# Performance work log

Hardware: AMD Instinct MI355X
Metric: run time of the kernel (lower is better)

Reference implementation:

```python
import jax, jax.numpy as jnp
import numpy as np

B, S, BERT_H = 8, 512, 432
NL, HD = 12, 64
H = NL * HD  # 768
NEG = -1e12

def _lin(k, i, o):
    return jax.random.normal(k, (i, o), jnp.float32) * 0.02

def setup_inputs():
    key = jax.random.key(0)
    ks = jax.random.split(key, 12)
    return {
        "bert_hidden": jax.random.normal(ks[0], (B, S, BERT_H), jnp.float32),
        "attention_mask": jnp.ones((B, S), jnp.float32),
        "dense_w": _lin(ks[1], BERT_H, H), "dense_b": jnp.zeros((H,)),
        "sat_qw": _lin(ks[2], H, H), "sat_qb": jnp.zeros((H,)),
        "sat_kw": _lin(ks[3], H, H), "sat_kb": jnp.zeros((H,)),
        "sat_vw": _lin(ks[4], H, H), "sat_vb": jnp.zeros((H,)),
        "sat_ow": _lin(ks[5], H, H), "sat_ob": jnp.zeros((H,)),
        "rel_qw": _lin(ks[6], H, H), "rel_qb": jnp.zeros((H,)),
        "rel_kw": _lin(ks[7], H, H), "rel_kb": jnp.zeros((H,)),
        "rel_vw": _lin(ks[8], H, H), "rel_vb": jnp.zeros((H,)),
        "rel_ow": _lin(ks[9], H, H), "rel_ob": jnp.zeros((H,)),
        "lns_w": jnp.ones((H,)), "lns_b": jnp.zeros((H,)),
        "lnr_w": jnp.ones((H,)), "lnr_b": jnp.zeros((H,)),
        "head_w": _lin(ks[10], H, 2 * HD), "head_b": jnp.zeros((2 * HD,)),
        "tail_w": _lin(ks[11], 2 * HD, 2 * NL), "tail_b": jnp.zeros((2 * NL,)),
    }

def _layernorm(x, w, b, eps=1e-12):
    u = x.mean(-1, keepdims=True)
    s = ((x - u) ** 2).mean(-1, keepdims=True)
    return w * (x - u) / jnp.sqrt(s + eps) + b

def _mha(q_in, k_in, v_in, wq, bq, wk, bk, wv, bv, wo, bo):
    # q_in: [N, Lq, H]; k_in/v_in: [N, Lk, H]; dropout is identity (eval)
    N, Lq, _ = q_in.shape
    Lk = k_in.shape[1]
    qh = (q_in @ wq + bq).reshape(N, Lq, NL, HD)
    kh = (k_in @ wk + bk).reshape(N, Lk, NL, HD)
    vh = (v_in @ wv + bv).reshape(N, Lk, NL, HD)
    scores = jnp.einsum('nqhd,nkhd->nhqk', qh, kh) / np.float32(np.sqrt(HD))
    probs = jax.nn.softmax(scores, axis=-1)
    ctx = jnp.einsum('nhqk,nkhd->nqhd', probs, vh).reshape(N, Lq, NL * HD)
    return ctx @ wo + bo + q_in

def _shift_back(x):
    # faithful torch cycle_shift(forward=False): circular roll left by 1
    return jnp.roll(x, -1, axis=1)

def _shift_fwd(x):
    # faithful to the torch sequential in-place loop in cycle_shift(forward=True):
    # out[0] = x[-1]; out[1:] = x[0] (each copy reads the already-overwritten slot)
    b, s, h = x.shape
    return jnp.concatenate([x[:, -1:, :], jnp.broadcast_to(x[:, :1, :], (b, s - 1, h))], axis=1)

def reference(bert_hidden, attention_mask, dense_w, dense_b,
              sat_qw, sat_qb, sat_kw, sat_kb, sat_vw, sat_vb, sat_ow, sat_ob,
              rel_qw, rel_qb, rel_kw, rel_kb, rel_vw, rel_vb, rel_ow, rel_ob,
              lns_w, lns_b, lnr_w, lnr_b, head_w, head_b, tail_w, tail_b):
    hidden0 = bert_hidden @ dense_w + dense_b  # [B,S,H]
    cs = hidden0
    center = cs.mean(axis=1)  # [B,H], avg_pool2d over seq dim
    for _ in range(2):
        before = _shift_back(cs)
        after = _shift_fwd(cs)
        center_exp = jnp.broadcast_to(center[:, None, :], cs.shape)
        concats = jnp.stack([before, cs, after, hidden0, center_exp], axis=2)  # [B,S,5,H]
        concats = concats.reshape(B * S, 5, H)
        q = cs.reshape(B * S, 1, H)
        sat = _mha(q, concats, concats, sat_qw, sat_qb, sat_kw, sat_kb, sat_vw, sat_vb, sat_ow, sat_ob)
        cs = _layernorm(jax.nn.relu(sat), lns_w, lns_b).reshape(B, S, H)
        cc = jnp.concatenate([center[:, None, :], cs], axis=1)  # [B,S+1,H]
        rel = _mha(center[:, None, :], cc, cc, rel_qw, rel_qb, rel_kw, rel_kb, rel_vw, rel_vb, rel_ow, rel_ob)
        center = _layernorm(jax.nn.relu(rel), lnr_w, lnr_b)[:, 0, :]
    outputs = cs @ head_w + head_b  # [B,S,2*HD]
    qw, kw = outputs[..., ::2], outputs[..., 1::2]  # [B,S,HD]
    pos = jnp.arange(S, dtype=jnp.float32)
    inv = jnp.power(10000.0, -2.0 * jnp.arange(HD // 2, dtype=jnp.float32) / HD)
    ang = pos[:, None] * inv[None, :]  # [S,HD//2]
    pe = jnp.stack([jnp.sin(ang), jnp.cos(ang)], axis=-1).reshape(S, HD)
    cos_pos = jnp.repeat(pe[:, 1::2], 2, axis=-1)  # [S,HD]
    sin_pos = jnp.repeat(pe[:, ::2], 2, axis=-1)
    def rot(x):
        x2 = jnp.stack([-x[..., 1::2], x[..., ::2]], axis=-1).reshape(x.shape)
        return x * cos_pos + x2 * sin_pos
    qw, kw = rot(qw), rot(kw)
    logits = jnp.einsum('bmd,bnd->bmn', qw, kw) / np.float32(np.sqrt(HD))  # [B,S,S]
    bias = jnp.einsum('bnh->bhn', outputs @ tail_w + tail_b) / 2.0  # [B,2*NL,S]
    logits = logits[:, None, :, :] + bias[:, ::2, None, :] + bias[:, 1::2, :, None]  # [B,NL,S,S]
    m1 = attention_mask[:, None, :, None]
    logits = logits * m1 + NEG * (1.0 - m1)
    m2 = attention_mask[:, None, None, :]
    logits = logits * m2 + NEG * (1.0 - m2)
    tril = jnp.tril(jnp.ones((S, S), logits.dtype), k=-1)
    return logits - tril * 1e12
```

## Files before the change

kernel.cpp:

```cpp
#include <hip/hip_runtime.h>
#include <cstdint>
#include <cstddef>

#define HH 768
#define SS 512
#define NBATCH 8
#define NLH 12
#define HDIM 64
#define BSROWS 4096
static constexpr float NEGV = -1000000000000.0f;

typedef unsigned short ushort_t;
typedef __attribute__((ext_vector_type(4))) float fx4;
typedef __attribute__((ext_vector_type(8))) short sx8;

__device__ __forceinline__ ushort_t f2bf(float f) {
  uint32_t u = __float_as_uint(f);
  uint32_t r = (u + 0x7FFFu + ((u >> 16) & 1u)) >> 16;
  return (ushort_t)r;
}
__device__ __forceinline__ float bf2f(ushort_t h) {
  return __uint_as_float(((uint32_t)h) << 16);
}
__device__ __forceinline__ float2 ldbf2(const ushort_t* p) {
  uint32_t u = *(const uint32_t*)p;
  return make_float2(__uint_as_float(u << 16), __uint_as_float(u & 0xffff0000u));
}

__device__ __forceinline__ void async_copy16(void* lds, const void* g) {
  __builtin_amdgcn_global_load_lds(
      (const __attribute__((address_space(1))) void*)g,
      (__attribute__((address_space(3))) void*)lds, 16, 0, 0);
}

__device__ __forceinline__ void gemm_core(
    char* arena, int bid, int nwg, int nx,
    const ushort_t* __restrict__ A, int lda,
    const ushort_t* __restrict__ B, int ldb,
    const float* __restrict__ bias,
    const ushort_t* __restrict__ resb,
    ushort_t* __restrict__ Cb, int ldo,
    ushort_t* __restrict__ Cb2, int ldo2, int nsplit, int K,
    float* __restrict__ colmean)
{
  ushort_t* As = (ushort_t*)arena;
  ushort_t* Bs = (ushort_t*)(arena + 16384);
  const int tid = threadIdx.x;
  const int q = nwg >> 3;
  const int xcd = bid & 7, sidx = bid >> 3;
  const int swz = xcd * q + sidx;
  const int bm = (swz / nx) * 128;
  const int bn = (swz % nx) * 128;
  const int l = tid & 63;
  const int w = tid >> 6;
  const int wr = w >> 1, wc = w & 1;
  const int r8 = tid >> 3;
  const int sl = tid & 7;

  fx4 acc[4][4];
#pragma unroll
  for (int m = 0; m < 4; ++m)
#pragma unroll
    for (int n = 0; n < 4; ++n) acc[m][n] = (fx4)0.f;

  for (int k0 = 0; k0 < K; k0 += 64) {
#pragma unroll
    for (int i = 0; i < 4; ++i) {
      int row = i * 32 + r8;
      int srcs = sl ^ (row & 7);
      async_copy16((char*)As + i * 4096 + tid * 16,
                   A + (size_t)(bm + row) * lda + k0 + srcs * 8);
    }
#pragma unroll
    for (int i = 0; i < 4; ++i) {
      int row = i * 32 + r8;
      int srcs = sl ^ (row & 7);
      async_copy16((char*)Bs + i * 4096 + tid * 16,
                   B + (size_t)(bn + row) * ldb + k0 + srcs * 8);
    }
    __syncthreads();
#pragma unroll
    for (int kk = 0; kk < 2; ++kk) {
      sx8 av[4], bv[4];
      const int so = (l >> 4) + kk * 4;
#pragma unroll
      for (int m = 0; m < 4; ++m) {
        int r = wr * 64 + m * 16 + (l & 15);
        av[m] = *(const sx8*)((const char*)As + r * 128 + ((so ^ (r & 7)) * 16));
      }
#pragma unroll
      for (int n = 0; n < 4; ++n) {
        int r = wc * 64 + n * 16 + (l & 15);
        bv[n] = *(const sx8*)((const char*)Bs + r * 128 + ((so ^ (r & 7)) * 16));
      }
#pragma unroll
      for (int m = 0; m < 4; ++m)
#pragma unroll
        for (int n = 0; n < 4; ++n)
          acc[m][n] = __builtin_amdgcn_mfma_f32_16x16x32_bf16(av[m], bv[n], acc[m][n], 0, 0, 0);
    }
    __syncthreads();
  }

  const bool second = (bn >= nsplit);
  ushort_t* dst = second ? Cb2 : Cb;
  const int ld = second ? ldo2 : ldo;
  const int csub = second ? nsplit : 0;
  const int cr0 = bm + wr * 64 + (l >> 4) * 4;
  const int cc0 = bn + wc * 64 + (l & 15);
#pragma unroll
  for (int m = 0; m < 4; ++m) {
#pragma unroll
    for (int n = 0; n < 4; ++n) {
      int col = cc0 + n * 16;
      float bcol = bias[col];
#pragma unroll
      for (int j = 0; j < 4; ++j) {
        int row = cr0 + m * 16 + j;
        size_t off = (size_t)row * ld + (col - csub);
        float v = acc[m][n][j] + bcol;
        if (resb) v += bf2f(resb[off]);
        dst[off] = f2bf(v);
      }
    }
  }

  if (colmean) {
    float* scr = (float*)arena;
    const int cid = wr * 4 + (l >> 4);
#pragma unroll
    for (int n = 0; n < 4; ++n) {
      int colL = wc * 64 + n * 16 + (l & 15);
      float t = 16.0f * bias[bn + colL];
#pragma unroll
      for (int m = 0; m < 4; ++m)
#pragma unroll
        for (int j = 0; j < 4; ++j) t += acc[m][n][j];
      scr[cid * 128 + colL] = t;
    }
    __syncthreads();
    if (tid < 128) {
      float scol = 0.f;
#pragma unroll
      for (int c = 0; c < 8; ++c) scol += scr[c * 128 + tid];
      atomicAdd(&colmean[(bm >> 9) * HH + bn + tid], scol * (1.0f / 512.0f));
    }
  }
}

struct SmallJob { const float* W; const float* bias; const float* res; float* C; };
struct SmallJobs { SmallJob j[5]; };

__device__ __forceinline__ void skinny_core(
    char* arena, int colblk,
    const float* __restrict__ A, const float* __restrict__ W,
    const float* __restrict__ bias, const float* __restrict__ res, float* __restrict__ C)
{
  float* As = (float*)arena;
  float* part = (float*)(arena + 24576);
  const int tid = threadIdx.x;
#pragma unroll
  for (int i = 0; i < 6; ++i) {
    int idx = tid * 4 + i * 1024;
    *(float4*)&As[idx] = *(const float4*)(A + idx);
  }
  __syncthreads();
  const int c = tid & 31;
  const int col = (colblk << 5) + c;
  const int ks = tid >> 5;
  const float* Wp = W + (size_t)(ks * 96) * HH + col;
  float acc[8] = {};
#pragma unroll 8
  for (int k = 0; k < 96; ++k) {
    float wv = Wp[(size_t)k * HH];
    const float* ap = &As[ks * 96 + k];
#pragma unroll
    for (int m = 0; m < 8; ++m)
      acc[m] = fmaf(ap[m * HH], wv, acc[m]);
  }
#pragma unroll
  for (int m = 0; m < 8; ++m)
    part[ks * 256 + m * 32 + c] = acc[m];
  __syncthreads();
  const int m = tid >> 5;
  const int c2 = tid & 31;
  float s = 0.f;
#pragma unroll
  for (int k = 0; k < 8; ++k) s += part[k * 256 + m * 32 + c2];
  const int outcol = (colblk << 5) + c2;
  float v = s + bias[outcol];
  if (res) v += res[(size_t)m * HH + outcol];
  C[(size_t)m * HH + outcol] = v;
}

__device__ __forceinline__ void rel_core(
    char* arena, int b, int h,
    const float* __restrict__ Qr, const float* __restrict__ Krc, const ushort_t* __restrict__ Kr,
    const float* __restrict__ Vrc, const ushort_t* __restrict__ Vr,
    const float* __restrict__ rel_ow, float* __restrict__ relo)
{
  float* qs = (float*)arena;
  float* sc = (float*)(arena + 256);
  float* part = (float*)(arena + 2560);
  float* redm = (float*)(arena + 3584);
  float* redsum = (float*)(arena + 3600);
  float* ctxs = (float*)(arena + 3616);
  int t = threadIdx.x, lane = t & 63, wave = t >> 6;
  if (t < 64) qs[t] = Qr[b * HH + h * HDIM + t];
  __syncthreads();
  for (int j = t; j < 513; j += 256) {
    float acc = 0.f;
    if (j == 0) {
      const float* kp = Krc + b * HH + h * HDIM;
#pragma unroll
      for (int d = 0; d < HDIM; ++d) acc = fmaf(qs[d], kp[d], acc);
    } else {
      const sx8* kv = (const sx8*)(Kr + (size_t)(b * SS + j - 1) * 1536 + h * HDIM);
#pragma unroll
      for (int dq = 0; dq < 8; ++dq) {
        sx8 v = kv[dq];
#pragma unroll
        for (int e = 0; e < 8; ++e)
          acc = fmaf(qs[dq * 8 + e], bf2f((ushort_t)v[e]), acc);
      }
    }
    sc[j] = acc * 0.125f;
  }
  __syncthreads();
  float m = -1e30f;
  for (int j = t; j < 513; j += 256) m = fmaxf(m, sc[j]);
#pragma unroll
  for (int d = 1; d < 64; d <<= 1) m = fmaxf(m, __shfl_xor(m, d));
  if (lane == 0) redm[wave] = m;
  __syncthreads();
  m = fmaxf(fmaxf(redm[0], redm[1]), fmaxf(redm[2], redm[3]));
  float lsum = 0.f;
  for (int j = t; j < 513; j += 256) { float e = __expf(sc[j] - m); sc[j] = e; lsum += e; }
#pragma unroll
  for (int d = 1; d < 64; d <<= 1) lsum += __shfl_xor(lsum, d);
  if (lane == 0) redsum[wave] = lsum;
  __syncthreads();
  float total = redsum[0] + redsum[1] + redsum[2] + redsum[3];
  float accv = 0.f;
#pragma unroll 8
  for (int j = wave; j < 513; j += 4) {
    float vv = (j == 0) ? Vrc[b * HH + h * HDIM + lane]
                        : bf2f(Vr[(size_t)(b * SS + j - 1) * 1536 + h * HDIM + lane]);
    accv = fmaf(sc[j], vv, accv);
  }
  part[wave * 64 + lane] = accv;
  __syncthreads();
  if (wave == 0)
    ctxs[lane] = (part[0 * 64 + lane] + part[1 * 64 + lane] +
                  part[2 * 64 + lane] + part[3 * 64 + lane]) / total;
  __syncthreads();
  for (int c = t; c < HH; c += 256) {
    const float* Wp = rel_ow + (size_t)(h * 64) * HH + c;
    float a0 = 0.f, a1 = 0.f, a2 = 0.f, a3 = 0.f;
#pragma unroll
    for (int d = 0; d < 64; d += 4) {
      a0 = fmaf(ctxs[d + 0], Wp[(size_t)(d + 0) * HH], a0);
      a1 = fmaf(ctxs[d + 1], Wp[(size_t)(d + 1) * HH], a1);
      a2 = fmaf(ctxs[d + 2], Wp[(size_t)(d + 2) * HH], a2);
      a3 = fmaf(ctxs[d + 3], Wp[(size_t)(d + 3) * HH], a3);
    }
    atomicAdd(&relo[b * HH + c], (a0 + a1) + (a2 + a3));
  }
}

__global__ __launch_bounds__(256) void gemm_bf16(
    const ushort_t* __restrict__ A, int lda,
    const ushort_t* __restrict__ B, int ldb,
    const float* __restrict__ bias,
    const ushort_t* __restrict__ resb,
    ushort_t* __restrict__ Cb, int ldo,
    ushort_t* __restrict__ Cb2, int ldo2, int nsplit, int K, int nx,
    float* __restrict__ colmean)
{
  __shared__ char arena[32768];
  gemm_core(arena, blockIdx.x, gridDim.x, nx, A, lda, B, ldb, bias, resb,
            Cb, ldo, Cb2, ldo2, nsplit, K, colmean);
}

__global__ __launch_bounds__(256) void qkv_center(
    const ushort_t* __restrict__ A, const ushort_t* __restrict__ B,
    const float* __restrict__ bias, ushort_t* __restrict__ Cb,
    SmallJobs jobs, const float* __restrict__ center)
{
  __shared__ char arena[32768];
  if (blockIdx.x < 576) {
    gemm_core(arena, blockIdx.x, 576, 18, A, HH, B, HH, bias, nullptr,
              Cb, 2304, nullptr, 0, 1 << 30, HH, nullptr);
  } else {
    int vb = blockIdx.x - 576;
    SmallJob jb = jobs.j[vb / 24];
    skinny_core(arena, vb % 24, center, jb.W, jb.bias, jb.res, jb.C);
  }
}

__global__ __launch_bounds__(256) void qkv2_rel(
    const ushort_t* __restrict__ A, const ushort_t* __restrict__ B,
    const float* __restrict__ bias, ushort_t* __restrict__ Cb,
    const float* __restrict__ Qr, const float* __restrict__ Krc,
    const ushort_t* __restrict__ Kr,
    const float* __restrict__ Vrc, const ushort_t* __restrict__ Vr,
    const float* __restrict__ rel_ow, float* __restrict__ relo)
{
  __shared__ char arena[32768];
  if (blockIdx.x < 576) {
    gemm_core(arena, blockIdx.x, 576, 18, A, HH, B, HH, bias, nullptr,
              Cb, 2304, nullptr, 0, 1 << 30, HH, nullptr);
  } else {
    int v = blockIdx.x - 576;
    rel_core(arena, v / 12, v % 12, Qr, Krc, Kr, Vrc, Vr, rel_ow, relo);
  }
}

struct SmallJobs2 { SmallJob j[2]; };
__global__ __launch_bounds__(256) void skinny_ln(
    const float* __restrict__ relo, const float* __restrict__ rel_ob,
    const float* __restrict__ center,
    const float* __restrict__ lw, const float* __restrict__ lb,
    SmallJobs2 jobs)
{
  __shared__ float As[8 * HH];
  __shared__ float part[8 * 8 * 32];
  const int tid = threadIdx.x;
  const SmallJob job = jobs.j[blockIdx.y];
#pragma unroll
  for (int i = 0; i < 6; ++i) {
    int idx = tid * 4 + i * 1024;
    int row = idx / HH;
    int col = idx - row * HH;
    float4 r4 = *(const float4*)(relo + idx);
    float4 o4 = *(const float4*)(rel_ob + col);
    float4 c4 = *(const float4*)(center + idx);
    As[idx + 0] = r4.x + o4.x + c4.x;
    As[idx + 1] = r4.y + o4.y + c4.y;
    As[idx + 2] = r4.z + o4.z + c4.z;
    As[idx + 3] = r4.w + o4.w + c4.w;
  }
  __syncthreads();
  {
    const int row = tid >> 5, lc = tid & 31;
    float s = 0.f, sq = 0.f;
#pragma unroll
    for (int e = 0; e < 24; ++e) {
      float x = fmaxf(As[row * HH + lc * 24 + e], 0.f);
      s += x; sq += x * x;
    }
#pragma unroll
    for (int d = 1; d < 32; d <<= 1) { s += __shfl_xor(s, d); sq += __shfl_xor(sq, d); }
    float mean = s * (1.0f / HH);
    float var = sq * (1.0f / HH) - mean * mean;
    float rstd = rsqrtf(var + 1e-12f);
#pragma unroll
    for (int e = 0; e < 24; ++e) {
      int cc = lc * 24 + e;
      float x = fmaxf(As[row * HH + cc], 0.f);
      As[row * HH + cc] = lw[cc] * (x - mean) * rstd + lb[cc];
    }
  }
  __syncthreads();
  const int c = tid & 31;
  const int col = (blockIdx.x << 5) + c;
  const int ks = tid >> 5;
  const float* Wp = job.W + (size_t)(ks * 96) * HH + col;
  float acc[8] = {};
#pragma unroll 8
  for (int k = 0; k < 96; ++k) {
    float wv = Wp[(size_t)k * HH];
    const float* ap = &As[ks * 96 + k];
#pragma unroll
    for (int m = 0; m < 8; ++m)
      acc[m] = fmaf(ap[m * HH], wv, acc[m]);
  }
#pragma unroll
  for (int m = 0; m < 8; ++m)
    part[ks * 256 + m * 32 + c] = acc[m];
  __syncthreads();
  const int m = tid >> 5;
  const int c2 = tid & 31;
  float s2 = 0.f;
#pragma unroll
  for (int k = 0; k < 8; ++k) s2 += part[k * 256 + m * 32 + c2];
  const int outcol = (blockIdx.x << 5) + c2;
  job.C[(size_t)m * HH + outcol] = s2 + job.bias[outcol];
}

__global__ __launch_bounds__(256) void head_fused(
    const ushort_t* __restrict__ Araw,
    const float* __restrict__ lnw, const float* __restrict__ lnb,
    const ushort_t* __restrict__ B,
    const float* __restrict__ head_b,
    const float* __restrict__ tail_w,
    const float* __restrict__ tail_b,
    float* __restrict__ qw, float* __restrict__ kw,
    float* __restrict__ bias2)
{
  __shared__ ushort_t As[16 * 64];
  __shared__ ushort_t Bs[128 * 64];
  __shared__ float tile[16][130];
  __shared__ float invt[32];
  __shared__ float2 rst[16];
  const int tid = threadIdx.x;
  const int bm = blockIdx.x * 16;
  const int l = tid & 63;
  const int w = tid >> 6;
  const int r8 = tid >> 3;
  const int sl = tid & 7;

  if (tid < 32) invt[tid] = powf(10000.0f, -(float)tid / 32.0f);

  {
    int row = tid >> 4, part = tid & 15;
    const ushort_t* rp = Araw + (size_t)(bm + row) * HH + part * 48;
    float s = 0.f, sq = 0.f;
#pragma unroll
    for (int c = 0; c < 6; ++c) {
      sx8 v = *(const sx8*)(rp + c * 8);
#pragma unroll
      for (int e = 0; e < 8; ++e) {
        float x = fmaxf(bf2f((ushort_t)v[e]), 0.f);
        s += x; sq += x * x;
      }
    }
#pragma unroll
    for (int d = 1; d < 16; d <<= 1) { s += __shfl_xor(s, d); sq += __shfl_xor(sq, d); }
    if (part == 0) {
      float mean = s * (1.0f / HH);
      float var = sq * (1.0f / HH) - mean * mean;
      rst[row] = make_float2(mean, rsqrtf(var + 1e-12f));
    }
  }
  __syncthreads();

  fx4 acc[2];
  acc[0] = (fx4)0.f; acc[1] = (fx4)0.f;

  for (int k0 = 0; k0 < HH; k0 += 64) {
#pragma unroll
    for (int i = 0; i < 4; ++i) {
      int row = i * 32 + r8;
      int srcs = sl ^ (row & 7);
      async_copy16((char*)Bs + i * 4096 + tid * 16,
                   B + (size_t)row * HH + k0 + srcs * 8);
    }
    if (tid < 128) {
      int row = tid >> 3;
      int slot = sl ^ (row & 7);
      int gk = k0 + slot * 8;
      sx8 v = *(const sx8*)(Araw + (size_t)(bm + row) * HH + gk);
      float4 w0 = *(const float4*)(lnw + gk);
      float4 w1 = *(const float4*)(lnw + gk + 4);
      float4 b0 = *(const float4*)(lnb + gk);
      float4 b1 = *(const float4*)(lnb + gk + 4);
      float wv[8] = {w0.x, w0.y, w0.z, w0.w, w1.x, w1.y, w1.z, w1.w};
      float bv[8] = {b0.x, b0.y, b0.z, b0.w, b1.x, b1.y, b1.z, b1.w};
      float2 mr = rst[row];
      sx8 ov;
#pragma unroll
      for (int e = 0; e < 8; ++e) {
        float x = fmaxf(bf2f((ushort_t)v[e]), 0.f);
        ov[e] = (short)f2bf(fmaf((x - mr.x) * mr.y, wv[e], bv[e]));
      }
      *(sx8*)((char*)As + row * 128 + sl * 16) = ov;
    }
    __syncthreads();
#pragma unroll
    for (int kk = 0; kk < 2; ++kk) {
      const int so = (l >> 4) + kk * 4;
      int ra = l & 15;
      sx8 av = *(const sx8*)((const char*)As + ra * 128 + ((so ^ (ra & 7)) * 16));
#pragma unroll
      for (int n = 0; n < 2; ++n) {
        int r = w * 32 + n * 16 + (l & 15);
        sx8 bv = *(const sx8*)((const char*)Bs + r * 128 + ((so ^ (r & 7)) * 16));
        acc[n] = __builtin_amdgcn_mfma_f32_16x16x32_bf16(av, bv, acc[n], 0, 0, 0);
      }
    }
    __syncthreads();
  }

  {
    const int rr0 = (l >> 4) * 4;
#pragma unroll
    for (int n = 0; n < 2; ++n) {
      int col = w * 32 + n * 16 + (l & 15);
      float bcol = head_b[col];
#pragma unroll
      for (int j = 0; j < 4; ++j)
        tile[rr0 + j][col] = acc[n][j] + bcol;
    }
  }
  __syncthreads();

#pragma unroll
  for (int it = 0; it < 2; ++it) {
    int t = tid + it * 256;
    int r = t >> 5, i = t & 31;
    int s = (bm + r) & 511;
    float ang = (float)s * invt[i];
    float sn = sinf(ang), cn = cosf(ang);
    float q0 = tile[r][4 * i + 0], k0 = tile[r][4 * i + 1];
    float q1 = tile[r][4 * i + 2], k1 = tile[r][4 * i + 3];
    float* qp = qw + (size_t)(bm + r) * 64 + i * 2;
    float* kp = kw + (size_t)(bm + r) * 64 + i * 2;
    qp[0] = q0 * cn - q1 * sn; qp[1] = q1 * cn + q0 * sn;
    kp[0] = k0 * cn - k1 * sn; kp[1] = k1 * cn + k0 * sn;
  }
  for (int t = tid; t < 16 * 24; t += 256) {
    int r = t / 24, c = t % 24;
    float acc2 = tail_b[c];
#pragma unroll 16
    for (int k = 0; k < 128; ++k) acc2 = fmaf(tile[r][k], tail_w[k * 24 + c], acc2);
    bias2[(size_t)(bm + r) * 24 + c] = acc2 * 0.5f;
  }
}

struct TJob { const float* src; ushort_t* dst; int K, N, Kpad, rowOff; };
struct PrepArgs {
  TJob j[8];
  const float* bert; ushort_t* bert_bf;
  const float* rkb; const float* rvb; const float* sqb; const float* skb; const float* svb;
  float* b_merged;
  float* center;
  float* relo;
};
__global__ __launch_bounds__(256) void prep_all(PrepArgs pa)
{
  if (blockIdx.z < 8) {
    TJob jb = pa.j[blockIdx.z];
    int k0 = blockIdx.x * 32, n0 = blockIdx.y * 32;
    if (k0 >= jb.Kpad || n0 >= jb.N) return;
    __shared__ float t[32][33];
    int tx = threadIdx.x & 31, ty = threadIdx.x >> 5;
#pragma unroll
    for (int i = 0; i < 4; ++i) {
      int k = k0 + ty + i * 8;
      float v = 0.f;
      if (k < jb.K && n0 + tx < jb.N) v = jb.src[(size_t)k * jb.N + n0 + tx];
      t[ty + i * 8][tx] = v;
    }
    __syncthreads();
#pragma unroll
    for (int i = 0; i < 4; ++i) {
      int n = n0 + ty + i * 8;
      int k = k0 + tx;
      if (n < jb.N && k < jb.Kpad)
        jb.dst[(size_t)(jb.rowOff + n) * jb.Kpad + k] = f2bf(t[tx][ty + i * 8]);
    }
  } else {
    const int NB = BSROWS * 448;
    const int total = NB + 3840 + 2 * NBATCH * HH;
    int start = (blockIdx.y * 24 + blockIdx.x) * 256 + threadIdx.x;
    for (int i = start; i < total; i += 24 * 24 * 256) {
      if (i < NB) {
        int r = i / 448, c = i % 448;
        pa.bert_bf[i] = (c < 432) ? f2bf(pa.bert[(size_t)r * 432 + c]) : (ushort_t)0;
      } else if (i < NB + 3840) {
        int c = i - NB;
        float v;
        if (c < 768) v = pa.rkb[c];
        else if (c < 1536) v = pa.rvb[c - 768];
        else if (c < 2304) v = pa.sqb[c - 1536];
        else if (c < 3072) v = pa.skb[c - 2304];
        else v = pa.svb[c - 3072];
        pa.b_merged[c] = v;
      } else if (i < NB + 3840 + NBATCH * HH) {
        pa.center[i - NB - 3840] = 0.f;
      } else {
        pa.relo[i - NB - 3840 - NBATCH * HH] = 0.f;
      }
    }
  }
}

__global__ __launch_bounds__(256) void sat_attn(
    const ushort_t* __restrict__ Qc, const ushort_t* __restrict__ Kc,
    const ushort_t* __restrict__ Vc, int ldq,
    const ushort_t* __restrict__ Kh0, const ushort_t* __restrict__ Vh0, int ldh,
    const float* __restrict__ Kcen, const float* __restrict__ Vcen,
    ushort_t* __restrict__ ctxb)
{
  int i = ((blockIdx.x & 7) << 9) | (blockIdx.x >> 3);
  int b = i >> 9, s = i & 511;
  int lane = threadIdx.x & 63;
  int wave = threadIdx.x >> 6;
  size_t rb = (size_t)(b * SS + ((s + 1) & 511));
  size_t rs = (size_t)i;
  size_t ra = (size_t)(b * SS + (s == 0 ? (SS - 1) : 0));
  size_t rc = (size_t)b * HH;
  const int half = lane >> 5;
  const int d0 = (lane & 31) * 2;
#pragma unroll
  for (int it = 0; it < 2; ++it) {
    int p = wave + 4 * it;
    if (p >= 6) break;
    int off = (2 * p + half) * HDIM + d0;
    float2 q  = ldbf2(Qc + rs * ldq + off);
    float2 kb = ldbf2(Kc + rb * ldq + off);
    float2 ks = ldbf2(Kc + rs * ldq + off);
    float2 ka = ldbf2(Kc + ra * ldq + off);
    float2 kh = ldbf2(Kh0 + rs * ldh + off);
    float2 kc = *(const float2*)(Kcen + rc + off);
    float s0 = q.x * kb.x + q.y * kb.y;
    float s1 = q.x * ks.x + q.y * ks.y;
    float s2 = q.x * ka.x + q.y * ka.y;
    float s3 = q.x * kh.x + q.y * kh.y;
    float s4 = q.x * kc.x + q.y * kc.y;
#pragma unroll
    for (int d = 1; d < 32; d <<= 1) {
      s0 += __shfl_xor(s0, d); s1 += __shfl_xor(s1, d); s2 += __shfl_xor(s2, d);
      s3 += __shfl_xor(s3, d); s4 += __shfl_xor(s4, d);
    }
    const float sc = 0.125f;
    s0 *= sc; s1 *= sc; s2 *= sc; s3 *= sc; s4 *= sc;
    float mx = fmaxf(fmaxf(fmaxf(s0, s1), fmaxf(s2, s3)), s4);
    float e0 = __expf(s0 - mx), e1 = __expf(s1 - mx), e2 = __expf(s2 - mx);
    float e3 = __expf(s3 - mx), e4 = __expf(s4 - mx);
    float inv = 1.f / (e0 + e1 + e2 + e3 + e4);
    float2 vb = ldbf2(Vc + rb * ldq + off);
    float2 vs = ldbf2(Vc + rs * ldq + off);
    float2 va = ldbf2(Vc + ra * ldq + off);
    float2 vh = ldbf2(Vh0 + rs * ldh + off);
    float2 vc = *(const float2*)(Vcen + rc + off);
    float vx = e0 * vb.x + e1 * vs.x + e2 * va.x + e3 * vh.x + e4 * vc.x;
    float vy = e0 * vb.y + e1 * vs.y + e2 * va.y + e3 * vh.y + e4 * vc.y;
    uint32_t o = (uint32_t)f2bf(vx * inv) | ((uint32_t)f2bf(vy * inv) << 16);
    *(uint32_t*)(ctxb + rs * HH + off) = o;
  }
}

__global__ __launch_bounds__(256) void relu_ln_bf(
    const ushort_t* __restrict__ x, const float* __restrict__ w, const float* __restrict__ b,
    ushort_t* __restrict__ ybf)
{
  int row = blockIdx.x;
  const ushort_t* xr = x + (size_t)row * HH;
  float v[3];
  float sum = 0.f, sumsq = 0.f;
#pragma unroll
  for (int j = 0; j < 3; ++j) {
    float t = bf2f(xr[threadIdx.x + j * 256]);
    t = fmaxf(t, 0.f);
    v[j] = t;
    sum += t; sumsq += t * t;
  }
#pragma unroll
  for (int d = 1; d < 64; d <<= 1) { sum += __shfl_xor(sum, d); sumsq += __shfl_xor(sumsq, d); }
  __shared__ float ws_[4], wsq_[4];
  int wave = threadIdx.x >> 6, lane = threadIdx.x & 63;
  if (lane == 0) { ws_[wave] = sum; wsq_[wave] = sumsq; }
  __syncthreads();
  sum = ws_[0] + ws_[1] + ws_[2] + ws_[3];
  sumsq = wsq_[0] + wsq_[1] + wsq_[2] + wsq_[3];
  float mean = sum * (1.0f / HH);
  float var = sumsq * (1.0f / HH) - mean * mean;
  float rstd = rsqrtf(var + 1e-12f);
#pragma unroll
  for (int j = 0; j < 3; ++j) {
    int cidx = threadIdx.x + j * 256;
    float o = w[cidx] * (v[j] - mean) * rstd + b[cidx];
    ybf[(size_t)row * HH + cidx] = f2bf(o);
  }
}

__global__ __launch_bounds__(256) void final_kernel(
    const float* __restrict__ qw, const float* __restrict__ kw,
    const float* __restrict__ bias2, const float* __restrict__ mask,
    float* __restrict__ out)
{
  int b = blockIdx.z;
  int mt = blockIdx.y * 32;
  int nt = blockIdx.x * 32;
  __shared__ float qs[32][68];
  __shared__ float ks[32][68];
  int t = threadIdx.x;
  {
    int idx = t * 8;
    int r = idx >> 6, c = idx & 63;
    const float* sq = qw + (size_t)(b * SS + mt + r) * 64 + c;
    const float* sk = kw + (size_t)(b * SS + nt + r) * 64 + c;
    *(float4*)&qs[r][c]     = *(const float4*)(sq);
    *(float4*)&qs[r][c + 4] = *(const float4*)(sq + 4);
    *(float4*)&ks[r][c]     = *(const float4*)(sk);
    *(float4*)&ks[r][c + 4] = *(const float4*)(sk + 4);
  }
  __syncthreads();
  int m = t >> 3;
  int n0 = (t & 7) * 4;
  float d0 = 0.f, d1 = 0.f, d2 = 0.f, d3 = 0.f;
#pragma unroll
  for (int d = 0; d < 64; d += 4) {
    float4 qv = *(const float4*)&qs[m][d];
    float4 k0 = *(const float4*)&ks[n0 + 0][d];
    float4 k1 = *(const float4*)&ks[n0 + 1][d];
    float4 k2 = *(const float4*)&ks[n0 + 2][d];
    float4 k3 = *(const float4*)&ks[n0 + 3][d];
    d0 += qv.x * k0.x + qv.y * k0.y + qv.z * k0.z + qv.w * k0.w;
    d1 += qv.x * k1.x + qv.y * k1.y + qv.z * k1.z + qv.w * k1.w;
    d2 += qv.x * k2.x + qv.y * k2.y + qv.z * k2.z + qv.w * k2.w;
    d3 += qv.x * k3.x + qv.y * k3.y + qv.z * k3.z + qv.w * k3.w;
  }
  int gm = mt + m;
  int gn = nt + n0;
  d0 *= 0.125f; d1 *= 0.125f; d2 *= 0.125f; d3 *= 0.125f;
  float mm = mask[b * SS + gm];
  float mn0 = mask[b * SS + gn + 0];
  float mn1 = mask[b * SS + gn + 1];
  float mn2 = mask[b * SS + gn + 2];
  float mn3 = mask[b * SS + gn + 3];
  const float* bmp  = bias2 + (size_t)(b * SS + gm) * 24;
  const float* bnp0 = bias2 + (size_t)(b * SS + gn + 0) * 24;
  const float* bnp1 = bias2 + (size_t)(b * SS + gn + 1) * 24;
  const float* bnp2 = bias2 + (size_t)(b * SS + gn + 2) * 24;
  const float* bnp3 = bias2 + (size_t)(b * SS + gn + 3) * 24;
#pragma unroll
  for (int h = 0; h < NLH; ++h) {
    float tb = bmp[2 * h + 1];
    float v0 = d0 + bnp0[2 * h] + tb;
    float v1 = d1 + bnp1[2 * h] + tb;
    float v2 = d2 + bnp2[2 * h] + tb;
    float v3 = d3 + bnp3[2 * h] + tb;
    v0 = v0 * mm + NEGV * (1.f - mm); v1 = v1 * mm + NEGV * (1.f - mm);
    v2 = v2 * mm + NEGV * (1.f - mm); v3 = v3 * mm + NEGV * (1.f - mm);
    v0 = v0 * mn0 + NEGV * (1.f - mn0); v1 = v1 * mn1 + NEGV * (1.f - mn1);
    v2 = v2 * mn2 + NEGV * (1.f - mn2); v3 = v3 * mn3 + NEGV * (1.f - mn3);
    if (gm > gn + 0) v0 -= 1000000000000.0f;
    if (gm > gn + 1) v1 -= 1000000000000.0f;
    if (gm > gn + 2) v2 -= 1000000000000.0f;
    if (gm > gn + 3) v3 -= 1000000000000.0f;
    float4 o = make_float4(v0, v1, v2, v3);
    *(float4*)(out + ((((size_t)(b * NLH + h)) * SS + gm) * SS + gn)) = o;
  }
}

extern "C" void kernel_launch(void* const* d_in, const int* in_sizes, int n_in,
                              void* d_out, int out_size, void* d_ws, size_t ws_size,
                              hipStream_t stream)
{
  const float* bert    = (const float*)d_in[0];
  const float* amask   = (const float*)d_in[1];
  const float* dense_w = (const float*)d_in[2];
  const float* dense_b = (const float*)d_in[3];
  const float* sat_qw  = (const float*)d_in[4];
  const float* sat_qb  = (const float*)d_in[5];
  const float* sat_kw  = (const float*)d_in[6];
  const float* sat_kb  = (const float*)d_in[7];
  const float* sat_vw  = (const float*)d_in[8];
  const float* sat_vb  = (const float*)d_in[9];
  const float* sat_ow  = (const float*)d_in[10];
  const float* sat_ob  = (const float*)d_in[11];
  const float* rel_qw  = (const float*)d_in[12];
  const float* rel_qb  = (const float*)d_in[13];
  const float* rel_kw  = (const float*)d_in[14];
  const float* rel_kb  = (const float*)d_in[15];
  const float* rel_vw  = (const float*)d_in[16];
  const float* rel_vb  = (const float*)d_in[17];
  const float* rel_ow  = (const float*)d_in[18];
  const float* rel_ob  = (const float*)d_in[19];
  const float* lns_w   = (const float*)d_in[20];
  const float* lns_b   = (const float*)d_in[21];
  const float* lnr_w   = (const float*)d_in[22];
  const float* lnr_b   = (const float*)d_in[23];
  const float* head_w  = (const float*)d_in[24];
  const float* head_b  = (const float*)d_in[25];
  const float* tail_w  = (const float*)d_in[26];
  const float* tail_b  = (const float*)d_in[27];

  float* out = (float*)d_out;
  char*  ws  = (char*)d_ws;

  size_t off = 0;
  auto alloc = [&](size_t bytes) { char* p = ws + off; off += (bytes + 255) & ~(size_t)255; return p; };
  ushort_t* bert_bf   = (ushort_t*)alloc((size_t)BSROWS * 448 * 2);
  ushort_t* Wt_dense  = (ushort_t*)alloc((size_t)768 * 448 * 2);
  ushort_t* Wt_big    = (ushort_t*)alloc((size_t)3840 * 768 * 2);
  ushort_t* Wt_satow  = (ushort_t*)alloc((size_t)768 * 768 * 2);
  ushort_t* Wt_head   = (ushort_t*)alloc((size_t)128 * 768 * 2);
  ushort_t* hidden0_bf= (ushort_t*)alloc((size_t)BSROWS * HH * 2);
  ushort_t* ctx_bf    = (ushort_t*)alloc((size_t)BSROWS * HH * 2);
  ushort_t* csA_bf    = (ushort_t*)alloc((size_t)BSROWS * HH * 2);
  float* b_merged = (float*)alloc(3840 * 4);
  float* center   = (float*)alloc(6144 * 4);
  float* Kcen     = (float*)alloc(6144 * 4);
  float* Vcen     = (float*)alloc(6144 * 4);
  float* Qr       = (float*)alloc(6144 * 4);
  float* Krc      = (float*)alloc(6144 * 4);
  float* Vrc      = (float*)alloc(6144 * 4);
  float* relo     = (float*)alloc(6144 * 4);
  float* bias2    = (float*)alloc((size_t)BSROWS * 24 * 4);
  float* qwbuf    = (float*)alloc((size_t)BSROWS * 64 * 4);
  float* kwbuf    = (float*)alloc((size_t)BSROWS * 64 * 4);

  ushort_t* QKV1_bf = (ushort_t*)out;
  ushort_t* tmp1_bf = QKV1_bf + (size_t)BSROWS * 2304;
  ushort_t* KrVr_bf = tmp1_bf + (size_t)BSROWS * 768;
  ushort_t* QKV2_bf = KrVr_bf + (size_t)BSROWS * 1536;
  ushort_t* tmp2_bf = tmp1_bf;

  dim3 blk(256);

  {
    PrepArgs pa;
    pa.j[0] = { dense_w, Wt_dense, 432, 768, 448, 0 };
    pa.j[1] = { rel_kw,  Wt_big,   768, 768, 768, 0 };
    pa.j[2] = { rel_vw,  Wt_big,   768, 768, 768, 768 };
    pa.j[3] = { sat_qw,  Wt_big,   768, 768, 768, 1536 };
    pa.j[4] = { sat_kw,  Wt_big,   768, 768, 768, 2304 };
    pa.j[5] = { sat_vw,  Wt_big,   768, 768, 768, 3072 };
    pa.j[6] = { sat_ow,  Wt_satow, 768, 768, 768, 0 };
    pa.j[7] = { head_w,  Wt_head,  768, 128, 768, 0 };
    pa.bert = bert; pa.bert_bf = bert_bf;
    pa.rkb = rel_kb; pa.rvb = rel_vb; pa.sqb = sat_qb; pa.skb = sat_kb; pa.svb = sat_vb;
    pa.b_merged = b_merged; pa.center = center; pa.relo = relo;
    prep_all<<<dim3(24, 24, 9), blk, 0, stream>>>(pa);
  }

  gemm_bf16<<<dim3(192), blk, 0, stream>>>(bert_bf, 448, Wt_dense, 448, dense_b,
                                           nullptr, hidden0_bf, HH,
                                           nullptr, 0, 1 << 30, 448, 6, center);

  {
    SmallJobs jobs;
    jobs.j[0] = { sat_kw, sat_kb, nullptr, Kcen };
    jobs.j[1] = { sat_vw, sat_vb, nullptr, Vcen };
    jobs.j[2] = { rel_qw, rel_qb, nullptr, Qr };
    jobs.j[3] = { rel_kw, rel_kb, nullptr, Krc };
    jobs.j[4] = { rel_vw, rel_vb, nullptr, Vrc };
    qkv_center<<<dim3(696), blk, 0, stream>>>(hidden0_bf, Wt_big + (size_t)1536 * 768,
                                              b_merged + 1536, QKV1_bf, jobs, center);
  }
  sat_attn<<<BSROWS, 256, 0, stream>>>(QKV1_bf, QKV1_bf + 768, QKV1_bf + 1536, 2304,
                                       QKV1_bf + 768, QKV1_bf + 1536, 2304,
                                       Kcen, Vcen, ctx_bf);
  gemm_bf16<<<dim3(192), blk, 0, stream>>>(ctx_bf, HH, Wt_satow, HH, sat_ob,
                                           hidden0_bf, tmp1_bf, HH,
                                           nullptr, 0, 1 << 30, HH, 6, nullptr);
  relu_ln_bf<<<BSROWS, 256, 0, stream>>>(tmp1_bf, lns_w, lns_b, csA_bf);

  gemm_bf16<<<dim3(480), blk, 0, stream>>>(csA_bf, HH, Wt_big, HH, b_merged,
                                           nullptr, KrVr_bf, 1536,
                                           nullptr, 0, 1 << 30, HH, 12, nullptr);
  qkv2_rel<<<dim3(672), blk, 0, stream>>>(csA_bf, Wt_big + (size_t)1536 * 768,
                                          b_merged + 1536, QKV2_bf,
                                          Qr, Krc, KrVr_bf, Vrc, KrVr_bf + 768,
                                          rel_ow, relo);
  {
    SmallJobs2 jobs;
    jobs.j[0] = { sat_kw, sat_kb, nullptr, Kcen };
    jobs.j[1] = { sat_vw, sat_vb, nullptr, Vcen };
    skinny_ln<<<dim3(24, 2), blk, 0, stream>>>(relo, rel_ob, center, lnr_w, lnr_b, jobs);
  }
  sat_attn<<<BSROWS, 256, 0, stream>>>(QKV2_bf, QKV2_bf + 768, QKV2_bf + 1536, 2304,
                                       QKV1_bf + 768, QKV1_bf + 1536, 2304,
                                       Kcen, Vcen, ctx_bf);
  gemm_bf16<<<dim3(192), blk, 0, stream>>>(ctx_bf, HH, Wt_satow, HH, sat_ob,
                                           csA_bf, tmp2_bf, HH,
                                           nullptr, 0, 1 << 30, HH, 6, nullptr);
  head_fused<<<256, blk, 0, stream>>>(tmp2_bf, lns_w, lns_b, Wt_head, head_b,
                                      tail_w, tail_b, qwbuf, kwbuf, bias2);
  final_kernel<<<dim3(16, 16, 8), 256, 0, stream>>>(qwbuf, kwbuf, bias2, amask, out);
}
```

Baseline: 256.8 us.

## Fold rel K/V projections into query-side vectors, drop KrVr GEMM

Removes the 4096x1536 GEMM that materialised the rel-attention K and V projections. Scores are now computed as cs·(Wk·q) plus a bias term, using a per-(batch,head) folded vector built in extra blocks appended to the first sat_attn launch. The context is computed as (probs·cs)·Wv plus bias corrections. This trades a large MFMA GEMM for scalar dot products over cs inside the rel blocks, which now read the full 768-wide rows and run longer, so those blocks could become the tail of qkv2_rel.

Result: slower. 332.9 us (+29.7%).

```diff
diff --git a/kernel.cpp b/kernel.cpp
--- a/kernel.cpp
+++ b/kernel.cpp
@@ -39,8 +39,7 @@
     const ushort_t* __restrict__ B, int ldb,
     const float* __restrict__ bias,
     const ushort_t* __restrict__ resb,
-    ushort_t* __restrict__ Cb, int ldo,
-    ushort_t* __restrict__ Cb2, int ldo2, int nsplit, int K,
+    ushort_t* __restrict__ Cb, int ldo, int K,
     float* __restrict__ colmean)
 {
   ushort_t* As = (ushort_t*)arena;
@@ -102,10 +101,6 @@
     __syncthreads();
   }
 
-  const bool second = (bn >= nsplit);
-  ushort_t* dst = second ? Cb2 : Cb;
-  const int ld = second ? ldo2 : ldo;
-  const int csub = second ? nsplit : 0;
   const int cr0 = bm + wr * 64 + (l >> 4) * 4;
   const int cc0 = bn + wc * 64 + (l & 15);
 #pragma unroll
@@ -117,10 +112,10 @@
 #pragma unroll
       for (int j = 0; j < 4; ++j) {
         int row = cr0 + m * 16 + j;
-        size_t off = (size_t)row * ld + (col - csub);
+        size_t off = (size_t)row * ldo + col;
         float v = acc[m][n][j] + bcol;
         if (resb) v += bf2f(resb[off]);
-        dst[off] = f2bf(v);
+        Cb[off] = f2bf(v);
       }
     }
   }
@@ -193,76 +188,98 @@
   C[(size_t)m * HH + outcol] = v;
 }
 
-__device__ __forceinline__ void rel_core(
+__device__ __forceinline__ void rel_core2(
     char* arena, int b, int h,
-    const float* __restrict__ Qr, const float* __restrict__ Krc, const ushort_t* __restrict__ Kr,
-    const float* __restrict__ Vrc, const ushort_t* __restrict__ Vr,
+    const ushort_t* __restrict__ cs,
+    const float* __restrict__ wtil, const float* __restrict__ qkb,
+    const float* __restrict__ Qr, const float* __restrict__ Krc,
+    const float* __restrict__ Vrc,
+    const float* __restrict__ rel_vw, const float* __restrict__ rel_vb,
     const float* __restrict__ rel_ow, float* __restrict__ relo)
 {
-  float* qs = (float*)arena;
-  float* sc = (float*)(arena + 256);
-  float* part = (float*)(arena + 2560);
-  float* redm = (float*)(arena + 3584);
-  float* redsum = (float*)(arena + 3600);
-  float* ctxs = (float*)(arena + 3616);
-  int t = threadIdx.x, lane = t & 63, wave = t >> 6;
-  if (t < 64) qs[t] = Qr[b * HH + h * HDIM + t];
-  __syncthreads();
-  for (int j = t; j < 513; j += 256) {
+  float* wt    = (float*)arena;
+  float* p     = (float*)(arena + 3072);
+  float* ctil  = (float*)(arena + 5376);
+  float* red   = (float*)(arena + 8448);
+  float* ctx   = (float*)(arena + 8576);
+  float* part4 = (float*)(arena + 8832);
+  const int tid = threadIdx.x, lane = tid & 63, wave = tid >> 6;
+
+  for (int k = tid; k < HH; k += 256) wt[k] = wtil[(size_t)(b * 12 + h) * HH + k];
+  __syncthreads();
+  const float qk = qkb[b * 12 + h];
+#pragma unroll
+  for (int jj = 0; jj < 2; ++jj) {
+    int j = 1 + tid + jj * 256;
+    const sx8* cp = (const sx8*)(cs + ((size_t)(b * SS) + (j - 1)) * HH);
+    float s0 = 0.f, s1 = 0.f;
+    for (int k8 = 0; k8 < 96; k8 += 2) {
+      sx8 v0 = cp[k8], v1 = cp[k8 + 1];
+#pragma unroll
+      for (int e = 0; e < 8; ++e) {
+        s0 = fmaf(bf2f((ushort_t)v0[e]), wt[k8 * 8 + e], s0);
+        s1 = fmaf(bf2f((ushort_t)v1[e]), wt[k8 * 8 + 8 + e], s1);
+      }
+    }
+    p[j] = s0 + s1 + qk;
+  }
+  if (tid < 64) {
+    float s0 = Qr[b * HH + h * 64 + tid] * Krc[b * HH + h * 64 + tid];
+#pragma unroll
+    for (int d = 1; d < 64; d <<= 1) s0 += __shfl_xor(s0, d);
+    if (tid == 0) p[0] = s0 * 0.125f;
+  }
+  __syncthreads();
+  float m = -1e30f;
+  for (int j = tid; j < 513; j += 256) m = fmaxf(m, p[j]);
+#pragma unroll
+  for (int d = 1; d < 64; d <<= 1) m = fmaxf(m, __shfl_xor(m, d));
+  if (lane == 0) red[wave] = m;
+  __syncthreads();
+  m = fmaxf(fmaxf(red[0], red[1]), fmaxf(red[2], red[3]));
+  float ls = 0.f;
+  for (int j = tid; j < 513; j += 256) { float e = __expf(p[j] - m); p[j] = e; ls += e; }
+#pragma unroll
+  for (int d = 1; d < 64; d <<= 1) ls += __shfl_xor(ls, d);
+  if (lane == 0) red[4 + wave] = ls;
+  __syncthreads();
+  float inv = 1.f / (red[4] + red[5] + red[6] + red[7]);
+  for (int j = tid; j < 513; j += 256) p[j] *= inv;
+  __syncthreads();
+#pragma unroll
+  for (int kk = 0; kk < 3; ++kk) {
+    int k = tid + kk * 256;
     float acc = 0.f;
-    if (j == 0) {
-      const float* kp = Krc + b * HH + h * HDIM;
-#pragma unroll
-      for (int d = 0; d < HDIM; ++d) acc = fmaf(qs[d], kp[d], acc);
-    } else {
-      const sx8* kv = (const sx8*)(Kr + (size_t)(b * SS + j - 1) * 1536 + h * HDIM);
-#pragma unroll
-      for (int dq = 0; dq < 8; ++dq) {
-        sx8 v = kv[dq];
-#pragma unroll
-        for (int e = 0; e < 8; ++e)
-          acc = fmaf(qs[dq * 8 + e], bf2f((ushort_t)v[e]), acc);
-      }
-    }
-    sc[j] = acc * 0.125f;
-  }
-  __syncthreads();
-  float m = -1e30f;
-  for (int j = t; j < 513; j += 256) m = fmaxf(m, sc[j]);
-#pragma unroll
-  for (int d = 1; d < 64; d <<= 1) m = fmaxf(m, __shfl_xor(m, d));
-  if (lane == 0) redm[wave] = m;
-  __syncthreads();
-  m = fmaxf(fmaxf(redm[0], redm[1]), fmaxf(redm[2], redm[3]));
-  float lsum = 0.f;
-  for (int j = t; j < 513; j += 256) { float e = __expf(sc[j] - m); sc[j] = e; lsum += e; }
-#pragma unroll
-  for (int d = 1; d < 64; d <<= 1) lsum += __shfl_xor(lsum, d);
-  if (lane == 0) redsum[wave] = lsum;
-  __syncthreads();
-  float total = redsum[0] + redsum[1] + redsum[2] + redsum[3];
-  float accv = 0.f;
+    const ushort_t* cp = cs + (size_t)(b * SS) * HH + k;
 #pragma unroll 8
-  for (int j = wave; j < 513; j += 4) {
-    float vv = (j == 0) ? Vrc[b * HH + h * HDIM + lane]
-                        : bf2f(Vr[(size_t)(b * SS + j - 1) * 1536 + h * HDIM + lane]);
-    accv = fmaf(sc[j], vv, accv);
-  }
-  part[wave * 64 + lane] = accv;
-  __syncthreads();
-  if (wave == 0)
-    ctxs[lane] = (part[0 * 64 + lane] + part[1 * 64 + lane] +
-                  part[2 * 64 + lane] + part[3 * 64 + lane]) / total;
-  __syncthreads();
-  for (int c = t; c < HH; c += 256) {
+    for (int j = 1; j <= 512; ++j)
+      acc = fmaf(p[j], bf2f(cp[(size_t)(j - 1) * HH]), acc);
+    ctil[k] = acc;
+  }
+  __syncthreads();
+  {
+    int d = tid & 63, qq = tid >> 6;
+    float acc = 0.f;
+    for (int k = qq * 192; k < qq * 192 + 192; ++k)
+      acc = fmaf(ctil[k], rel_vw[(size_t)k * HH + h * 64 + d], acc);
+    part4[qq * 64 + d] = acc;
+  }
+  __syncthreads();
+  if (tid < 64) {
+    float s = part4[tid] + part4[64 + tid] + part4[128 + tid] + part4[192 + tid];
+    float p0 = p[0];
+    ctx[tid] = s + (1.f - p0) * rel_vb[h * 64 + tid] + p0 * Vrc[b * HH + h * 64 + tid];
+  }
+  __syncthreads();
+  for (int c = tid; c < HH; c += 256) {
     const float* Wp = rel_ow + (size_t)(h * 64) * HH + c;
     float a0 = 0.f, a1 = 0.f, a2 = 0.f, a3 = 0.f;
 #pragma unroll
     for (int d = 0; d < 64; d += 4) {
-      a0 = fmaf(ctxs[d + 0], Wp[(size_t)(d + 0) * HH], a0);
-      a1 = fmaf(ctxs[d + 1], Wp[(size_t)(d + 1) * HH], a1);
-      a2 = fmaf(ctxs[d + 2], Wp[(size_t)(d + 2) * HH], a2);
-      a3 = fmaf(ctxs[d + 3], Wp[(size_t)(d + 3) * HH], a3);
+      a0 = fmaf(ctx[d + 0], Wp[(size_t)(d + 0) * HH], a0);
+      a1 = fmaf(ctx[d + 1], Wp[(size_t)(d + 1) * HH], a1);
+      a2 = fmaf(ctx[d + 2], Wp[(size_t)(d + 2) * HH], a2);
+      a3 = fmaf(ctx[d + 3], Wp[(size_t)(d + 3) * HH], a3);
     }
     atomicAdd(&relo[b * HH + c], (a0 + a1) + (a2 + a3));
   }
@@ -273,13 +290,12 @@
     const ushort_t* __restrict__ B, int ldb,
     const float* __restrict__ bias,
     const ushort_t* __restrict__ resb,
-    ushort_t* __restrict__ Cb, int ldo,
-    ushort_t* __restrict__ Cb2, int ldo2, int nsplit, int K, int nx,
+    ushort_t* __restrict__ Cb, int ldo, int K, int nx,
     float* __restrict__ colmean)
 {
   __shared__ char arena[32768];
   gemm_core(arena, blockIdx.x, gridDim.x, nx, A, lda, B, ldb, bias, resb,
-            Cb, ldo, Cb2, ldo2, nsplit, K, colmean);
+            Cb, ldo, K, colmean);
 }
 
 __global__ __launch_bounds__(256) void qkv_center(
@@ -290,7 +306,7 @@
   __shared__ char arena[32768];
   if (blockIdx.x < 576) {
     gemm_core(arena, blockIdx.x, 576, 18, A, HH, B, HH, bias, nullptr,
-              Cb, 2304, nullptr, 0, 1 << 30, HH, nullptr);
+              Cb, 2304, HH, nullptr);
   } else {
     int vb = blockIdx.x - 576;
     SmallJob jb = jobs.j[vb / 24];
@@ -301,18 +317,20 @@
 __global__ __launch_bounds__(256) void qkv2_rel(
     const ushort_t* __restrict__ A, const ushort_t* __restrict__ B,
     const float* __restrict__ bias, ushort_t* __restrict__ Cb,
+    const float* __restrict__ wtil, const float* __restrict__ qkb,
     const float* __restrict__ Qr, const float* __restrict__ Krc,
-    const ushort_t* __restrict__ Kr,
-    const float* __restrict__ Vrc, const ushort_t* __restrict__ Vr,
+    const float* __restrict__ Vrc,
+    const float* __restrict__ rel_vw, const float* __restrict__ rel_vb,
     const float* __restrict__ rel_ow, float* __restrict__ relo)
 {
   __shared__ char arena[32768];
   if (blockIdx.x < 576) {
     gemm_core(arena, blockIdx.x, 576, 18, A, HH, B, HH, bias, nullptr,
-              Cb, 2304, nullptr, 0, 1 << 30, HH, nullptr);
+              Cb, 2304, HH, nullptr);
   } else {
     int v = blockIdx.x - 576;
-    rel_core(arena, v / 12, v % 12, Qr, Krc, Kr, Vrc, Vr, rel_ow, relo);
+    rel_core2(arena, v / 12, v % 12, A, wtil, qkb, Qr, Krc, Vrc,
+              rel_vw, rel_vb, rel_ow, relo);
   }
 }
 
@@ -520,16 +538,16 @@
 
 struct TJob { const float* src; ushort_t* dst; int K, N, Kpad, rowOff; };
 struct PrepArgs {
-  TJob j[8];
+  TJob j[6];
   const float* bert; ushort_t* bert_bf;
-  const float* rkb; const float* rvb; const float* sqb; const float* skb; const float* svb;
+  const float* sqb; const float* skb; const float* svb;
   float* b_merged;
   float* center;
   float* relo;
 };
 __global__ __launch_bounds__(256) void prep_all(PrepArgs pa)
 {
-  if (blockIdx.z < 8) {
+  if (blockIdx.z < 6) {
     TJob jb = pa.j[blockIdx.z];
     int k0 = blockIdx.x * 32, n0 = blockIdx.y * 32;
     if (k0 >= jb.Kpad || n0 >= jb.N) return;
@@ -552,25 +570,23 @@
     }
   } else {
     const int NB = BSROWS * 448;
-    const int total = NB + 3840 + 2 * NBATCH * HH;
+    const int total = NB + 2304 + 2 * NBATCH * HH;
     int start = (blockIdx.y * 24 + blockIdx.x) * 256 + threadIdx.x;
     for (int i = start; i < total; i += 24 * 24 * 256) {
       if (i < NB) {
         int r = i / 448, c = i % 448;
         pa.bert_bf[i] = (c < 432) ? f2bf(pa.bert[(size_t)r * 432 + c]) : (ushort_t)0;
-      } else if (i < NB + 3840) {
+      } else if (i < NB + 2304) {
         int c = i - NB;
         float v;
-        if (c < 768) v = pa.rkb[c];
-        else if (c < 1536) v = pa.rvb[c - 768];
-        else if (c < 2304) v = pa.sqb[c - 1536];
-        else if (c < 3072) v = pa.skb[c - 2304];
-        else v = pa.svb[c - 3072];
+        if (c < 768) v = pa.sqb[c];
+        else if (c < 1536) v = pa.skb[c - 768];
+        else v = pa.svb[c - 1536];
         pa.b_merged[c] = v;
-      } else if (i < NB + 3840 + NBATCH * HH) {
-        pa.center[i - NB - 3840] = 0.f;
+      } else if (i < NB + 2304 + NBATCH * HH) {
+        pa.center[i - NB - 2304] = 0.f;
       } else {
-        pa.relo[i - NB - 3840 - NBATCH * HH] = 0.f;
+        pa.relo[i - NB - 2304 - NBATCH * HH] = 0.f;
       }
     }
   }
@@ -581,8 +597,39 @@
     const ushort_t* __restrict__ Vc, int ldq,
     const ushort_t* __restrict__ Kh0, const ushort_t* __restrict__ Vh0, int ldh,
     const float* __restrict__ Kcen, const float* __restrict__ Vcen,
-    ushort_t* __restrict__ ctxb)
-{
+    ushort_t* __restrict__ ctxb,
+    const float* __restrict__ Qr, const float* __restrict__ rel_kw,
+    const float* __restrict__ rel_kb,
+    float* __restrict__ wtil, float* __restrict__ qkb)
+{
+  __shared__ float qs[64];
+  if (blockIdx.x >= 4096) {
+    int v = blockIdx.x - 4096;
+    int b = v / 12, h = v % 12;
+    int tid = threadIdx.x;
+    if (tid < 64) qs[tid] = Qr[b * HH + h * 64 + tid];
+    __syncthreads();
+    if (tid < 64) {
+      float pq = qs[tid] * rel_kb[h * 64 + tid];
+#pragma unroll
+      for (int d = 1; d < 64; d <<= 1) pq += __shfl_xor(pq, d);
+      if (tid == 0) qkb[b * 12 + h] = pq * 0.125f;
+    }
+#pragma unroll
+    for (int kk = 0; kk < 3; ++kk) {
+      int k = tid + kk * 256;
+      const float4* wp = (const float4*)(rel_kw + (size_t)k * HH + h * 64);
+      float s = 0.f;
+#pragma unroll
+      for (int d4 = 0; d4 < 16; ++d4) {
+        float4 wv = wp[d4];
+        s += wv.x * qs[d4 * 4 + 0] + wv.y * qs[d4 * 4 + 1]
+           + wv.z * qs[d4 * 4 + 2] + wv.w * qs[d4 * 4 + 3];
+      }
+      wtil[(size_t)(b * 12 + h) * HH + k] = s * 0.125f;
+    }
+    return;
+  }
   int i = ((blockIdx.x & 7) << 9) | (blockIdx.x >> 3);
   int b = i >> 9, s = i & 511;
   int lane = threadIdx.x & 63;
@@ -776,13 +823,13 @@
   auto alloc = [&](size_t bytes) { char* p = ws + off; off += (bytes + 255) & ~(size_t)255; return p; };
   ushort_t* bert_bf   = (ushort_t*)alloc((size_t)BSROWS * 448 * 2);
   ushort_t* Wt_dense  = (ushort_t*)alloc((size_t)768 * 448 * 2);
-  ushort_t* Wt_big    = (ushort_t*)alloc((size_t)3840 * 768 * 2);
+  ushort_t* Wt_big    = (ushort_t*)alloc((size_t)2304 * 768 * 2);
   ushort_t* Wt_satow  = (ushort_t*)alloc((size_t)768 * 768 * 2);
   ushort_t* Wt_head   = (ushort_t*)alloc((size_t)128 * 768 * 2);
   ushort_t* hidden0_bf= (ushort_t*)alloc((size_t)BSROWS * HH * 2);
   ushort_t* ctx_bf    = (ushort_t*)alloc((size_t)BSROWS * HH * 2);
   ushort_t* csA_bf    = (ushort_t*)alloc((size_t)BSROWS * HH * 2);
-  float* b_merged = (float*)alloc(3840 * 4);
+  float* b_merged = (float*)alloc(2304 * 4);
   float* center   = (float*)alloc(6144 * 4);
   float* Kcen     = (float*)alloc(6144 * 4);
   float* Vcen     = (float*)alloc(6144 * 4);
@@ -790,14 +837,15 @@
   float* Krc      = (float*)alloc(6144 * 4);
   float* Vrc      = (float*)alloc(6144 * 4);
   float* relo     = (float*)alloc(6144 * 4);
+  float* wtil     = (float*)alloc((size_t)96 * HH * 4);
+  float* qkb      = (float*)alloc(96 * 4);
   float* bias2    = (float*)alloc((size_t)BSROWS * 24 * 4);
   float* qwbuf    = (float*)alloc((size_t)BSROWS * 64 * 4);
   float* kwbuf    = (float*)alloc((size_t)BSROWS * 64 * 4);
 
   ushort_t* QKV1_bf = (ushort_t*)out;
   ushort_t* tmp1_bf = QKV1_bf + (size_t)BSROWS * 2304;
-  ushort_t* KrVr_bf = tmp1_bf + (size_t)BSROWS * 768;
-  ushort_t* QKV2_bf = KrVr_bf + (size_t)BSROWS * 1536;
+  ushort_t* QKV2_bf = tmp1_bf + (size_t)BSROWS * 768;
   ushort_t* tmp2_bf = tmp1_bf;
 
   dim3 blk(256);
@@ -805,22 +853,19 @@
   {
     PrepArgs pa;
     pa.j[0] = { dense_w, Wt_dense, 432, 768, 448, 0 };
-    pa.j[1] = { rel_kw,  Wt_big,   768, 768, 768, 0 };
-    pa.j[2] = { rel_vw,  Wt_big,   768, 768, 768, 768 };
-    pa.j[3] = { sat_qw,  Wt_big,   768, 768, 768, 1536 };
-    pa.j[4] = { sat_kw,  Wt_big,   768, 768, 768, 2304 };
-    pa.j[5] = { sat_vw,  Wt_big,   768, 768, 768, 3072 };
-    pa.j[6] = { sat_ow,  Wt_satow, 768, 768, 768, 0 };
-    pa.j[7] = { head_w,  Wt_head,  768, 128, 768, 0 };
+    pa.j[1] = { sat_qw,  Wt_big,   768, 768, 768, 0 };
+    pa.j[2] = { sat_kw,  Wt_big,   768, 768, 768, 768 };
+    pa.j[3] = { sat_vw,  Wt_big,   768, 768, 768, 1536 };
+    pa.j[4] = { sat_ow,  Wt_satow, 768, 768, 768, 0 };
+    pa.j[5] = { head_w,  Wt_head,  768, 128, 768, 0 };
     pa.bert = bert; pa.bert_bf = bert_bf;
-    pa.rkb = rel_kb; pa.rvb = rel_vb; pa.sqb = sat_qb; pa.skb = sat_kb; pa.svb = sat_vb;
+    pa.sqb = sat_qb; pa.skb = sat_kb; pa.svb = sat_vb;
     pa.b_merged = b_merged; pa.center = center; pa.relo = relo;
-    prep_all<<<dim3(24, 24, 9), blk, 0, stream>>>(pa);
+    prep_all<<<dim3(24, 24, 7), blk, 0, stream>>>(pa);
   }
 
   gemm_bf16<<<dim3(192), blk, 0, stream>>>(bert_bf, 448, Wt_dense, 448, dense_b,
-                                           nullptr, hidden0_bf, HH,
-                                           nullptr, 0, 1 << 30, 448, 6, center);
+                                           nullptr, hidden0_bf, HH, 448, 6, center);
 
   {
     SmallJobs jobs;
@@ -829,36 +874,32 @@
     jobs.j[2] = { rel_qw, rel_qb, nullptr, Qr };
     jobs.j[3] = { rel_kw, rel_kb, nullptr, Krc };
     jobs.j[4] = { rel_vw, rel_vb, nullptr, Vrc };
-    qkv_center<<<dim3(696), blk, 0, stream>>>(hidden0_bf, Wt_big + (size_t)1536 * 768,
-                                              b_merged + 1536, QKV1_bf, jobs, center);
-  }
-  sat_attn<<<BSROWS, 256, 0, stream>>>(QKV1_bf, QKV1_bf + 768, QKV1_bf + 1536, 2304,
-                                       QKV1_bf + 768, QKV1_bf + 1536, 2304,
-                                       Kcen, Vcen, ctx_bf);
+    qkv_center<<<dim3(696), blk, 0, stream>>>(hidden0_bf, Wt_big,
+                                              b_merged, QKV1_bf, jobs, center);
+  }
+  sat_attn<<<dim3(4192), 256, 0, stream>>>(QKV1_bf, QKV1_bf + 768, QKV1_bf + 1536, 2304,
+                                           QKV1_bf + 768, QKV1_bf + 1536, 2304,
+                                           Kcen, Vcen, ctx_bf,
+                                           Qr, rel_kw, rel_kb, wtil, qkb);
   gemm_bf16<<<dim3(192), blk, 0, stream>>>(ctx_bf, HH, Wt_satow, HH, sat_ob,
-                                           hidden0_bf, tmp1_bf, HH,
-                                           nullptr, 0, 1 << 30, HH, 6, nullptr);
+                                           hidden0_bf, tmp1_bf, HH, HH, 6, nullptr);
   relu_ln_bf<<<BSROWS, 256, 0, stream>>>(tmp1_bf, lns_w, lns_b, csA_bf);
 
-  gemm_bf16<<<dim3(480), blk, 0, stream>>>(csA_bf, HH, Wt_big, HH, b_merged,
-                                           nullptr, KrVr_bf, 1536,
-                                           nullptr, 0, 1 << 30, HH, 12, nullptr);
-  qkv2_rel<<<dim3(672), blk, 0, stream>>>(csA_bf, Wt_big + (size_t)1536 * 768,
-                                          b_merged + 1536, QKV2_bf,
-                                          Qr, Krc, KrVr_bf, Vrc, KrVr_bf + 768,
-                                          rel_ow, relo);
+  qkv2_rel<<<dim3(672), blk, 0, stream>>>(csA_bf, Wt_big, b_merged, QKV2_bf,
+                                          wtil, qkb, Qr, Krc, Vrc,
+                                          rel_vw, rel_vb, rel_ow, relo);
   {
     SmallJobs2 jobs;
     jobs.j[0] = { sat_kw, sat_kb, nullptr, Kcen };
     jobs.j[1] = { sat_vw, sat_vb, nullptr, Vcen };
     skinny_ln<<<dim3(24, 2), blk, 0, stream>>>(relo, rel_ob, center, lnr_w, lnr_b, jobs);
   }
-  sat_attn<<<BSROWS, 256, 0, stream>>>(QKV2_bf, QKV2_bf + 768, QKV2_bf + 1536, 2304,
-                                       QKV1_bf + 768, QKV1_bf + 1536, 2304,
-                                       Kcen, Vcen, ctx_bf);
+  sat_attn<<<dim3(4096), 256, 0, stream>>>(QKV2_bf, QKV2_bf + 768, QKV2_bf + 1536, 2304,
+                                           QKV1_bf + 768, QKV1_bf + 1536, 2304,
+                                           Kcen, Vcen, ctx_bf,
+                                           Qr, rel_kw, rel_kb, wtil, qkb);
   gemm_bf16<<<dim3(192), blk, 0, stream>>>(ctx_bf, HH, Wt_satow, HH, sat_ob,
-                                           csA_bf, tmp2_bf, HH,
-                                           nullptr, 0, 1 << 30, HH, 6, nullptr);
+                                           csA_bf, tmp2_bf, HH, HH, 6, nullptr);
   head_fused<<<256, blk, 0, stream>>>(tmp2_bf, lns_w, lns_b, Wt_head, head_b,
                                       tail_w, tail_b, qwbuf, kwbuf, bias2);
   final_kernel<<<dim3(16, 16, 8), 256, 0, stream>>>(qwbuf, kwbuf, bias2, amask, out);
```
